# Kernel tuning notes

Hardware: AMD Instinct MI355X
Metric: run time of the kernel (lower is better)

Reference implementation:

```python
import jax, jax.numpy as jnp
import numpy as np

D = 64  # hidden_dim


def _bn(x, gamma, beta):
    # eval-mode BatchNorm1d with running_mean=0, running_var=1 (fresh model)
    return gamma * x + beta


def _edge_conv(h, W, b, gamma, beta):
    # h: [B,N,D]; W: [2D,D] split into Wi (acts on x_i) and Wj (acts on x_j)
    Wi, Wj = W[:D], W[D:]
    ti = jnp.einsum('bnd,de->bne', h, Wi)  # [B,N,D] (i term)
    tj = jnp.einsum('bmd,de->bme', h, Wj)  # [B,N,D] (j term)
    # e[b,i,j,:] = x_i@Wi + x_j@Wj + b  -> relu -> BN -> max over j
    e = ti[:, :, None, :] + tj[:, None, :, :] + b  # [B,N,N,D]
    e = _bn(jax.nn.relu(e), gamma, beta)
    return e.max(axis=2)  # [B,N,D]


def setup_inputs() -> dict:
    key = jax.random.key(0)
    ks = jax.random.split(key, 16)
    s = lambda k, shp, sc: (jax.random.normal(k, shp, dtype=jnp.float32) * sc)
    inp = {
        'x': s(ks[0], (32, 256, 4), 1.0),
        'W1': s(ks[1], (4, D), 0.5), 'b1': s(ks[2], (D,), 0.1),
        'g1': 1.0 + s(ks[3], (D,), 0.1), 'beta1': s(ks[4], (D,), 0.1),
        'We1': s(ks[5], (2 * D, D), 0.1), 'be1': s(ks[6], (D,), 0.1),
        'ge1': 1.0 + s(ks[7], (D,), 0.1), 'betae1': s(ks[8], (D,), 0.1),
        'We2': s(ks[9], (2 * D, D), 0.1), 'be2': s(ks[10], (D,), 0.1),
        'ge2': 1.0 + s(ks[11], (D,), 0.1), 'betae2': s(ks[12], (D,), 0.1),
        'Wg1': s(ks[13], (2 * D, D), 0.1), 'bg1': s(ks[14], (D,), 0.1),
        'Wg2': s(ks[15], (D, 2), 0.1), 'bg2': jnp.zeros((2,), jnp.float32),
    }
    return inp


def reference(x, W1, b1, g1, beta1, We1, be1, ge1, betae1, We2, be2, ge2, betae2, Wg1, bg1, Wg2, bg2):
    # input MLP: Linear -> ReLU -> BN (eval)
    h = _bn(jax.nn.relu(x @ W1 + b1), g1, beta1)  # [B,N,D]
    h = _edge_conv(h, We1, be1, ge1, betae1)
    h = _edge_conv(h, We2, be2, ge2, betae2)
    x_mean = h.mean(axis=1)  # [B,D]
    x_max = h.max(axis=1)    # [B,D]
    xg = jnp.concatenate([x_mean, x_max], axis=-1)  # [B,2D]
    # global MLP (dropout is identity in eval)
    out = jax.nn.relu(xg @ Wg1 + bg1) @ Wg2 + bg2  # [B,2]
    return out
```

## Files before the change

### kernel.cpp

```cpp
#include <hip/hip_runtime.h>

#define NB 32
#define NN 256
#define DD 64
#define GG 4
#define NPB 64
#define FMAXV 3.402823466e+38f


__global__ __launch_bounds__(512) void k_conv1(
    const float* __restrict__ x,
    const float* __restrict__ W1,  const float* __restrict__ b1,
    const float* __restrict__ g1,  const float* __restrict__ beta1,
    const float* __restrict__ We1,
    float* __restrict__ TI, float* __restrict__ PMAX, float* __restrict__ PMIN)
{
    __shared__ float Hs[NPB * 65];
    const int b  = blockIdx.x >> 2;
    const int g  = blockIdx.x & 3;
    const int l  = threadIdx.x & 63;
    const int w  = __builtin_amdgcn_readfirstlane(threadIdx.x >> 6);
    const int n  = g * NPB + l;
    const int d0 = w * 8;

    {
        float4 xv = *(const float4*)(x + ((size_t)b * NN + n) * 4);
        float a[8];
#pragma unroll
        for (int j = 0; j < 8; ++j) a[j] = b1[d0 + j];
#pragma unroll
        for (int j = 0; j < 8; ++j) a[j] = fmaf(xv.x, W1[0 * DD + d0 + j], a[j]);
#pragma unroll
        for (int j = 0; j < 8; ++j) a[j] = fmaf(xv.y, W1[1 * DD + d0 + j], a[j]);
#pragma unroll
        for (int j = 0; j < 8; ++j) a[j] = fmaf(xv.z, W1[2 * DD + d0 + j], a[j]);
#pragma unroll
        for (int j = 0; j < 8; ++j) a[j] = fmaf(xv.w, W1[3 * DD + d0 + j], a[j]);
#pragma unroll
        for (int j = 0; j < 8; ++j)
            Hs[l * 65 + d0 + j] = g1[d0 + j] * fmaxf(a[j], 0.f) + beta1[d0 + j];
    }
    __syncthreads();

    float ti[8], tj[8];
#pragma unroll
    for (int j = 0; j < 8; ++j) { ti[j] = 0.f; tj[j] = 0.f; }
#pragma unroll
    for (int k = 0; k < DD; ++k) {
        const float hk = Hs[l * 65 + k];
        const float* wi = We1 + k * DD + d0;
        const float* wj = We1 + (DD + k) * DD + d0;
#pragma unroll
        for (int j = 0; j < 8; ++j) {
            ti[j] = fmaf(hk, wi[j], ti[j]);
            tj[j] = fmaf(hk, wj[j], tj[j]);
        }
    }
    {
        float* o = TI + ((size_t)(b * NN + n)) * DD + d0;
        *(float4*)(o)     = make_float4(ti[0], ti[1], ti[2], ti[3]);
        *(float4*)(o + 4) = make_float4(ti[4], ti[5], ti[6], ti[7]);
    }
    float mx[8], mn[8];
#pragma unroll
    for (int j = 0; j < 8; ++j) { mx[j] = tj[j]; mn[j] = tj[j]; }
#pragma unroll
    for (int m = 1; m < 64; m <<= 1) {
#pragma unroll
        for (int j = 0; j < 8; ++j) {
            mx[j] = fmaxf(mx[j], __shfl_xor(mx[j], m, 64));
            mn[j] = fminf(mn[j], __shfl_xor(mn[j], m, 64));
        }
    }
    float smx = mx[0], smn = mn[0];
#pragma unroll
    for (int j = 1; j < 8; ++j) {
        smx = (l == j) ? mx[j] : smx;
        smn = (l == j) ? mn[j] : smn;
    }
    if (l < 8) {
        PMAX[(b * GG + g) * DD + d0 + l] = smx;
        PMIN[(b * GG + g) * DD + d0 + l] = smn;
    }
}

__global__ __launch_bounds__(512) void k_conv2(
    const float* __restrict__ PMAXin, const float* __restrict__ PMINin,
    const float* __restrict__ beP, const float* __restrict__ geP,
    const float* __restrict__ bteP,
    const float* __restrict__ We,
    float* __restrict__ TI, float* __restrict__ PMAX, float* __restrict__ PMIN)
{
    __shared__ float Hs[NPB * 65];
    const int b  = blockIdx.x >> 2;
    const int g  = blockIdx.x & 3;
    const int l  = threadIdx.x & 63;
    const int w  = __builtin_amdgcn_readfirstlane(threadIdx.x >> 6);
    const int n  = g * NPB + l;
    const int d0 = w * 8;

    float rmax[8], rmin[8];
#pragma unroll
    for (int j = 0; j < 8; ++j) {
        rmax[j] = fmaxf(fmaxf(PMAXin[(b * GG + 0) * DD + d0 + j],
                              PMAXin[(b * GG + 1) * DD + d0 + j]),
                        fmaxf(PMAXin[(b * GG + 2) * DD + d0 + j],
                              PMAXin[(b * GG + 3) * DD + d0 + j]));
        rmin[j] = fminf(fminf(PMINin[(b * GG + 0) * DD + d0 + j],
                              PMINin[(b * GG + 1) * DD + d0 + j]),
                        fminf(PMINin[(b * GG + 2) * DD + d0 + j],
                              PMINin[(b * GG + 3) * DD + d0 + j]));
    }
    {
        const float* tip = TI + ((size_t)(b * NN + n)) * DD + d0;
        float4 t0 = *(const float4*)tip;
        float4 t1 = *(const float4*)(tip + 4);
        float tiv[8] = {t0.x, t0.y, t0.z, t0.w, t1.x, t1.y, t1.z, t1.w};
#pragma unroll
        for (int j = 0; j < 8; ++j) {
            float gv = geP[d0 + j];
            float sv = tiv[j] + (gv >= 0.f ? rmax[j] : rmin[j]) + beP[d0 + j];
            Hs[l * 65 + d0 + j] = gv * fmaxf(sv, 0.f) + bteP[d0 + j];
        }
    }
    __syncthreads();

    float ti[8], tj[8];
#pragma unroll
    for (int j = 0; j < 8; ++j) { ti[j] = 0.f; tj[j] = 0.f; }
#pragma unroll
    for (int k = 0; k < DD; ++k) {
        const float hk = Hs[l * 65 + k];
        const float* wi = We + k * DD + d0;
        const float* wj = We + (DD + k) * DD + d0;
#pragma unroll
        for (int j = 0; j < 8; ++j) {
            ti[j] = fmaf(hk, wi[j], ti[j]);
            tj[j] = fmaf(hk, wj[j], tj[j]);
        }
    }
    {
        float* o = TI + ((size_t)(b * NN + n)) * DD + d0;
        *(float4*)(o)     = make_float4(ti[0], ti[1], ti[2], ti[3]);
        *(float4*)(o + 4) = make_float4(ti[4], ti[5], ti[6], ti[7]);
    }
    float mx[8], mn[8];
#pragma unroll
    for (int j = 0; j < 8; ++j) { mx[j] = tj[j]; mn[j] = tj[j]; }
#pragma unroll
    for (int m = 1; m < 64; m <<= 1) {
#pragma unroll
        for (int j = 0; j < 8; ++j) {
            mx[j] = fmaxf(mx[j], __shfl_xor(mx[j], m, 64));
            mn[j] = fminf(mn[j], __shfl_xor(mn[j], m, 64));
        }
    }
    float smx = mx[0], smn = mn[0];
#pragma unroll
    for (int j = 1; j < 8; ++j) {
        smx = (l == j) ? mx[j] : smx;
        smn = (l == j) ? mn[j] : smn;
    }
    if (l < 8) {
        PMAX[(b * GG + g) * DD + d0 + l] = smx;
        PMIN[(b * GG + g) * DD + d0 + l] = smn;
    }
}

__global__ __launch_bounds__(512) void k_pool(
    const float* __restrict__ PMAXin, const float* __restrict__ PMINin,
    const float* __restrict__ beP, const float* __restrict__ geP,
    const float* __restrict__ bteP,
    const float* __restrict__ TI,
    float* __restrict__ PSUM, float* __restrict__ PMXP)
{
    const int b  = blockIdx.x >> 2;
    const int g  = blockIdx.x & 3;
    const int l  = threadIdx.x & 63;
    const int w  = __builtin_amdgcn_readfirstlane(threadIdx.x >> 6);
    const int n  = g * NPB + l;
    const int d0 = w * 8;

    float rmax[8], rmin[8];
#pragma unroll
    for (int j = 0; j < 8; ++j) {
        rmax[j] = fmaxf(fmaxf(PMAXin[(b * GG + 0) * DD + d0 + j],
                              PMAXin[(b * GG + 1) * DD + d0 + j]),
                        fmaxf(PMAXin[(b * GG + 2) * DD + d0 + j],
                              PMAXin[(b * GG + 3) * DD + d0 + j]));
        rmin[j] = fminf(fminf(PMINin[(b * GG + 0) * DD + d0 + j],
                              PMINin[(b * GG + 1) * DD + d0 + j]),
                        fminf(PMINin[(b * GG + 2) * DD + d0 + j],
                              PMINin[(b * GG + 3) * DD + d0 + j]));
    }
    float hv[8];
    {
        const float* tip = TI + ((size_t)(b * NN + n)) * DD + d0;
        float4 t0 = *(const float4*)tip;
        float4 t1 = *(const float4*)(tip + 4);
        float tiv[8] = {t0.x, t0.y, t0.z, t0.w, t1.x, t1.y, t1.z, t1.w};
#pragma unroll
        for (int j = 0; j < 8; ++j) {
            float gv = geP[d0 + j];
            float sv = tiv[j] + (gv >= 0.f ? rmax[j] : rmin[j]) + beP[d0 + j];
            hv[j] = gv * fmaxf(sv, 0.f) + bteP[d0 + j];
        }
    }
    float sm[8], mx[8];
#pragma unroll
    for (int j = 0; j < 8; ++j) { sm[j] = hv[j]; mx[j] = hv[j]; }
#pragma unroll
    for (int m = 1; m < 64; m <<= 1) {
#pragma unroll
        for (int j = 0; j < 8; ++j) {
            sm[j] += __shfl_xor(sm[j], m, 64);
            mx[j] = fmaxf(mx[j], __shfl_xor(mx[j], m, 64));
        }
    }
    float ssm = sm[0], smx = mx[0];
#pragma unroll
    for (int j = 1; j < 8; ++j) {
        ssm = (l == j) ? sm[j] : ssm;
        smx = (l == j) ? mx[j] : smx;
    }
    if (l < 8) {
        PSUM[(b * GG + g) * DD + d0 + l] = ssm;
        PMXP[(b * GG + g) * DD + d0 + l] = smx;
    }
}

__global__ __launch_bounds__(128) void k_head(
    const float* __restrict__ PSUM, const float* __restrict__ PMXP,
    const float* __restrict__ Wg1, const float* __restrict__ bg1,
    const float* __restrict__ Wg2, const float* __restrict__ bg2,
    float* __restrict__ out)
{
    __shared__ float xg[2 * DD];
    __shared__ float hid[DD];
    const int b = blockIdx.x;
    const int t = threadIdx.x;
    if (t < 64) {
        float s = PSUM[(b * GG + 0) * DD + t] + PSUM[(b * GG + 1) * DD + t]
                + PSUM[(b * GG + 2) * DD + t] + PSUM[(b * GG + 3) * DD + t];
        xg[t] = s * (1.f / 256.f);
    } else {
        int d = t - 64;
        xg[64 + d] = fmaxf(fmaxf(PMXP[(b * GG + 0) * DD + d], PMXP[(b * GG + 1) * DD + d]),
                           fmaxf(PMXP[(b * GG + 2) * DD + d], PMXP[(b * GG + 3) * DD + d]));
    }
    __syncthreads();
    if (t < 64) {
        float a = bg1[t];
#pragma unroll
        for (int k = 0; k < 2 * DD; ++k) a = fmaf(xg[k], Wg1[k * DD + t], a);
        hid[t] = fmaxf(a, 0.f);
    }
    __syncthreads();
    if (t < 2) {
        float o = bg2[t];
#pragma unroll
        for (int j = 0; j < DD; ++j) o = fmaf(hid[j], Wg2[j * 2 + t], o);
        out[b * 2 + t] = o;
    }
}

extern "C" void kernel_launch(void* const* d_in, const int* in_sizes, int n_in,
                              void* d_out, int out_size, void* d_ws, size_t ws_size,
                              hipStream_t stream) {
    const float* x     = (const float*)d_in[0];
    const float* W1    = (const float*)d_in[1];
    const float* b1    = (const float*)d_in[2];
    const float* g1    = (const float*)d_in[3];
    const float* beta1 = (const float*)d_in[4];
    const float* We1   = (const float*)d_in[5];
    const float* be1   = (const float*)d_in[6];
    const float* ge1   = (const float*)d_in[7];
    const float* bte1  = (const float*)d_in[8];
    const float* We2   = (const float*)d_in[9];
    const float* be2   = (const float*)d_in[10];
    const float* ge2   = (const float*)d_in[11];
    const float* bte2  = (const float*)d_in[12];
    const float* Wg1   = (const float*)d_in[13];
    const float* bg1   = (const float*)d_in[14];
    const float* Wg2   = (const float*)d_in[15];
    const float* bg2   = (const float*)d_in[16];

    float* ws    = (float*)d_ws;
    float* TI    = ws;
    float* PMAX1 = ws + 524288;
    float* PMIN1 = ws + 532480;
    float* PMAX2 = ws + 540672;
    float* PMIN2 = ws + 548864;
    float* PSUM  = ws + 557056;
    float* PMXP  = ws + 565248;

    k_conv1<<<dim3(NB * GG), dim3(512), 0, stream>>>(
        x, W1, b1, g1, beta1, We1, TI, PMAX1, PMIN1);
    k_conv2<<<dim3(NB * GG), dim3(512), 0, stream>>>(
        PMAX1, PMIN1, be1, ge1, bte1, We2, TI, PMAX2, PMIN2);
    k_pool<<<dim3(NB * GG), dim3(512), 0, stream>>>(
        PMAX2, PMIN2, be2, ge2, bte2, TI, PSUM, PMXP);
    k_head<<<dim3(NB), dim3(128), 0, stream>>>(
        PSUM, PMXP, Wg1, bg1, Wg2, bg2, (float*)d_out);
}
```

Before: 121.3 us.

## Fuse all stages into one cooperative kernel with grid-wide syncs

Replaces the four kernel launches (conv1, conv2, pool, head) with a single cooperative kernel that separates stages with grid.sync(). The ti values now stay in registers between stages, so the TI round-trip through global memory is gone, and the head runs in the g==0 blocks. This removes launch gaps and global traffic. In exchange it pays for grid-barrier costs, needs all 128 blocks co-resident, and leaves 3/4 of the blocks idle during the head.

```diff
diff --git a/kernel.cpp b/kernel.cpp
--- a/kernel.cpp
+++ b/kernel.cpp
@@ -1,27 +1,89 @@
 #include <hip/hip_runtime.h>
+#include <hip/hip_cooperative_groups.h>
+
+namespace cg = cooperative_groups;
 
 #define NB 32
 #define NN 256
 #define DD 64
 #define GG 4
 #define NPB 64
-#define FMAXV 3.402823466e+38f
-
-
-__global__ __launch_bounds__(512) void k_conv1(
+
+
+__device__ __forceinline__ void matvec64(const float* Hrow, int d0,
+                                         const float* __restrict__ We,
+                                         float ti[8], float tj[8])
+{
+#pragma unroll
+    for (int j = 0; j < 8; ++j) { ti[j] = 0.f; tj[j] = 0.f; }
+#pragma unroll
+    for (int k = 0; k < DD; ++k) {
+        const float hk = Hrow[k];
+        const float* wi = We + k * DD + d0;
+        const float* wj = We + (DD + k) * DD + d0;
+#pragma unroll
+        for (int j = 0; j < 8; ++j) {
+            ti[j] = fmaf(hk, wi[j], ti[j]);
+            tj[j] = fmaf(hk, wj[j], tj[j]);
+        }
+    }
+}
+
+__device__ __forceinline__ void red_minmax_store(const float tj[8], int l,
+                                                 float* PMAX, float* PMIN, int idx)
+{
+    float mx[8], mn[8];
+#pragma unroll
+    for (int j = 0; j < 8; ++j) { mx[j] = tj[j]; mn[j] = tj[j]; }
+#pragma unroll
+    for (int m = 1; m < 64; m <<= 1) {
+#pragma unroll
+        for (int j = 0; j < 8; ++j) {
+            mx[j] = fmaxf(mx[j], __shfl_xor(mx[j], m, 64));
+            mn[j] = fminf(mn[j], __shfl_xor(mn[j], m, 64));
+        }
+    }
+    float smx = mx[0], smn = mn[0];
+#pragma unroll
+    for (int j = 1; j < 8; ++j) {
+        smx = (l == j) ? mx[j] : smx;
+        smn = (l == j) ? mn[j] : smn;
+    }
+    if (l < 8) {
+        PMAX[idx + l] = smx;
+        PMIN[idx + l] = smn;
+    }
+}
+
+__global__ __launch_bounds__(512, 2) void k_fused(
     const float* __restrict__ x,
     const float* __restrict__ W1,  const float* __restrict__ b1,
     const float* __restrict__ g1,  const float* __restrict__ beta1,
-    const float* __restrict__ We1,
-    float* __restrict__ TI, float* __restrict__ PMAX, float* __restrict__ PMIN)
+    const float* __restrict__ We1, const float* __restrict__ be1,
+    const float* __restrict__ ge1, const float* __restrict__ bte1,
+    const float* __restrict__ We2, const float* __restrict__ be2,
+    const float* __restrict__ ge2, const float* __restrict__ bte2,
+    const float* __restrict__ Wg1, const float* __restrict__ bg1,
+    const float* __restrict__ Wg2, const float* __restrict__ bg2,
+    float* ws, float* __restrict__ out)
 {
+    cg::grid_group grid = cg::this_grid();
     __shared__ float Hs[NPB * 65];
+
+    float* PMAX1 = ws;
+    float* PMIN1 = ws + 8192;
+    float* PMAX2 = ws + 16384;
+    float* PMIN2 = ws + 24576;
+    float* PSUM  = ws + 32768;
+    float* PMXP  = ws + 40960;
+
     const int b  = blockIdx.x >> 2;
     const int g  = blockIdx.x & 3;
     const int l  = threadIdx.x & 63;
     const int w  = __builtin_amdgcn_readfirstlane(threadIdx.x >> 6);
     const int n  = g * NPB + l;
     const int d0 = w * 8;
+    const int pidx = (b * GG + g) * DD + d0;
 
     {
         float4 xv = *(const float4*)(x + ((size_t)b * NN + n) * 4);
@@ -43,224 +105,104 @@
     __syncthreads();
 
     float ti[8], tj[8];
-#pragma unroll
-    for (int j = 0; j < 8; ++j) { ti[j] = 0.f; tj[j] = 0.f; }
-#pragma unroll
-    for (int k = 0; k < DD; ++k) {
-        const float hk = Hs[l * 65 + k];
-        const float* wi = We1 + k * DD + d0;
-        const float* wj = We1 + (DD + k) * DD + d0;
-#pragma unroll
-        for (int j = 0; j < 8; ++j) {
-            ti[j] = fmaf(hk, wi[j], ti[j]);
-            tj[j] = fmaf(hk, wj[j], tj[j]);
-        }
-    }
+    matvec64(Hs + l * 65, d0, We1, ti, tj);
+    red_minmax_store(tj, l, PMAX1, PMIN1, pidx);
+
+    grid.sync();
+
     {
-        float* o = TI + ((size_t)(b * NN + n)) * DD + d0;
-        *(float4*)(o)     = make_float4(ti[0], ti[1], ti[2], ti[3]);
-        *(float4*)(o + 4) = make_float4(ti[4], ti[5], ti[6], ti[7]);
-    }
-    float mx[8], mn[8];
-#pragma unroll
-    for (int j = 0; j < 8; ++j) { mx[j] = tj[j]; mn[j] = tj[j]; }
-#pragma unroll
-    for (int m = 1; m < 64; m <<= 1) {
-#pragma unroll
-        for (int j = 0; j < 8; ++j) {
-            mx[j] = fmaxf(mx[j], __shfl_xor(mx[j], m, 64));
-            mn[j] = fminf(mn[j], __shfl_xor(mn[j], m, 64));
-        }
-    }
-    float smx = mx[0], smn = mn[0];
-#pragma unroll
-    for (int j = 1; j < 8; ++j) {
-        smx = (l == j) ? mx[j] : smx;
-        smn = (l == j) ? mn[j] : smn;
-    }
-    if (l < 8) {
-        PMAX[(b * GG + g) * DD + d0 + l] = smx;
-        PMIN[(b * GG + g) * DD + d0 + l] = smn;
-    }
-}
-
-__global__ __launch_bounds__(512) void k_conv2(
-    const float* __restrict__ PMAXin, const float* __restrict__ PMINin,
-    const float* __restrict__ beP, const float* __restrict__ geP,
-    const float* __restrict__ bteP,
-    const float* __restrict__ We,
-    float* __restrict__ TI, float* __restrict__ PMAX, float* __restrict__ PMIN)
-{
-    __shared__ float Hs[NPB * 65];
-    const int b  = blockIdx.x >> 2;
-    const int g  = blockIdx.x & 3;
-    const int l  = threadIdx.x & 63;
-    const int w  = __builtin_amdgcn_readfirstlane(threadIdx.x >> 6);
-    const int n  = g * NPB + l;
-    const int d0 = w * 8;
-
-    float rmax[8], rmin[8];
-#pragma unroll
-    for (int j = 0; j < 8; ++j) {
-        rmax[j] = fmaxf(fmaxf(PMAXin[(b * GG + 0) * DD + d0 + j],
-                              PMAXin[(b * GG + 1) * DD + d0 + j]),
-                        fmaxf(PMAXin[(b * GG + 2) * DD + d0 + j],
-                              PMAXin[(b * GG + 3) * DD + d0 + j]));
-        rmin[j] = fminf(fminf(PMINin[(b * GG + 0) * DD + d0 + j],
-                              PMINin[(b * GG + 1) * DD + d0 + j]),
-                        fminf(PMINin[(b * GG + 2) * DD + d0 + j],
-                              PMINin[(b * GG + 3) * DD + d0 + j]));
-    }
+        float rmax[8], rmin[8];
+#pragma unroll
+        for (int j = 0; j < 8; ++j) {
+            const int base = b * GG * DD + d0 + j;
+            rmax[j] = fmaxf(fmaxf(PMAX1[base],          PMAX1[base + DD]),
+                            fmaxf(PMAX1[base + 2 * DD], PMAX1[base + 3 * DD]));
+            rmin[j] = fminf(fminf(PMIN1[base],          PMIN1[base + DD]),
+                            fminf(PMIN1[base + 2 * DD], PMIN1[base + 3 * DD]));
+        }
+#pragma unroll
+        for (int j = 0; j < 8; ++j) {
+            float gv = ge1[d0 + j];
+            float sv = ti[j] + (gv >= 0.f ? rmax[j] : rmin[j]) + be1[d0 + j];
+            Hs[l * 65 + d0 + j] = gv * fmaxf(sv, 0.f) + bte1[d0 + j];
+        }
+    }
+    __syncthreads();
+
+    matvec64(Hs + l * 65, d0, We2, ti, tj);
+    red_minmax_store(tj, l, PMAX2, PMIN2, pidx);
+
+    grid.sync();
+
     {
-        const float* tip = TI + ((size_t)(b * NN + n)) * DD + d0;
-        float4 t0 = *(const float4*)tip;
-        float4 t1 = *(const float4*)(tip + 4);
-        float tiv[8] = {t0.x, t0.y, t0.z, t0.w, t1.x, t1.y, t1.z, t1.w};
-#pragma unroll
-        for (int j = 0; j < 8; ++j) {
-            float gv = geP[d0 + j];
-            float sv = tiv[j] + (gv >= 0.f ? rmax[j] : rmin[j]) + beP[d0 + j];
-            Hs[l * 65 + d0 + j] = gv * fmaxf(sv, 0.f) + bteP[d0 + j];
-        }
-    }
-    __syncthreads();
-
-    float ti[8], tj[8];
-#pragma unroll
-    for (int j = 0; j < 8; ++j) { ti[j] = 0.f; tj[j] = 0.f; }
-#pragma unroll
-    for (int k = 0; k < DD; ++k) {
-        const float hk = Hs[l * 65 + k];
-        const float* wi = We + k * DD + d0;
-        const float* wj = We + (DD + k) * DD + d0;
-#pragma unroll
-        for (int j = 0; j < 8; ++j) {
-            ti[j] = fmaf(hk, wi[j], ti[j]);
-            tj[j] = fmaf(hk, wj[j], tj[j]);
-        }
-    }
-    {
-        float* o = TI + ((size_t)(b * NN + n)) * DD + d0;
-        *(float4*)(o)     = make_float4(ti[0], ti[1], ti[2], ti[3]);
-        *(float4*)(o + 4) = make_float4(ti[4], ti[5], ti[6], ti[7]);
-    }
-    float mx[8], mn[8];
-#pragma unroll
-    for (int j = 0; j < 8; ++j) { mx[j] = tj[j]; mn[j] = tj[j]; }
-#pragma unroll
-    for (int m = 1; m < 64; m <<= 1) {
-#pragma unroll
-        for (int j = 0; j < 8; ++j) {
-            mx[j] = fmaxf(mx[j], __shfl_xor(mx[j], m, 64));
-            mn[j] = fminf(mn[j], __shfl_xor(mn[j], m, 64));
-        }
-    }
-    float smx = mx[0], smn = mn[0];
-#pragma unroll
-    for (int j = 1; j < 8; ++j) {
-        smx = (l == j) ? mx[j] : smx;
-        smn = (l == j) ? mn[j] : smn;
-    }
-    if (l < 8) {
-        PMAX[(b * GG + g) * DD + d0 + l] = smx;
-        PMIN[(b * GG + g) * DD + d0 + l] = smn;
-    }
-}
-
-__global__ __launch_bounds__(512) void k_pool(
-    const float* __restrict__ PMAXin, const float* __restrict__ PMINin,
-    const float* __restrict__ beP, const float* __restrict__ geP,
-    const float* __restrict__ bteP,
-    const float* __restrict__ TI,
-    float* __restrict__ PSUM, float* __restrict__ PMXP)
-{
-    const int b  = blockIdx.x >> 2;
-    const int g  = blockIdx.x & 3;
-    const int l  = threadIdx.x & 63;
-    const int w  = __builtin_amdgcn_readfirstlane(threadIdx.x >> 6);
-    const int n  = g * NPB + l;
-    const int d0 = w * 8;
-
-    float rmax[8], rmin[8];
-#pragma unroll
-    for (int j = 0; j < 8; ++j) {
-        rmax[j] = fmaxf(fmaxf(PMAXin[(b * GG + 0) * DD + d0 + j],
-                              PMAXin[(b * GG + 1) * DD + d0 + j]),
-                        fmaxf(PMAXin[(b * GG + 2) * DD + d0 + j],
-                              PMAXin[(b * GG + 3) * DD + d0 + j]));
-        rmin[j] = fminf(fminf(PMINin[(b * GG + 0) * DD + d0 + j],
-                              PMINin[(b * GG + 1) * DD + d0 + j]),
-                        fminf(PMINin[(b * GG + 2) * DD + d0 + j],
-                              PMINin[(b * GG + 3) * DD + d0 + j]));
-    }
-    float hv[8];
-    {
-        const float* tip = TI + ((size_t)(b * NN + n)) * DD + d0;
-        float4 t0 = *(const float4*)tip;
-        float4 t1 = *(const float4*)(tip + 4);
-        float tiv[8] = {t0.x, t0.y, t0.z, t0.w, t1.x, t1.y, t1.z, t1.w};
-#pragma unroll
-        for (int j = 0; j < 8; ++j) {
-            float gv = geP[d0 + j];
-            float sv = tiv[j] + (gv >= 0.f ? rmax[j] : rmin[j]) + beP[d0 + j];
-            hv[j] = gv * fmaxf(sv, 0.f) + bteP[d0 + j];
-        }
-    }
-    float sm[8], mx[8];
-#pragma unroll
-    for (int j = 0; j < 8; ++j) { sm[j] = hv[j]; mx[j] = hv[j]; }
-#pragma unroll
-    for (int m = 1; m < 64; m <<= 1) {
-#pragma unroll
-        for (int j = 0; j < 8; ++j) {
-            sm[j] += __shfl_xor(sm[j], m, 64);
-            mx[j] = fmaxf(mx[j], __shfl_xor(mx[j], m, 64));
-        }
-    }
-    float ssm = sm[0], smx = mx[0];
-#pragma unroll
-    for (int j = 1; j < 8; ++j) {
-        ssm = (l == j) ? sm[j] : ssm;
-        smx = (l == j) ? mx[j] : smx;
-    }
-    if (l < 8) {
-        PSUM[(b * GG + g) * DD + d0 + l] = ssm;
-        PMXP[(b * GG + g) * DD + d0 + l] = smx;
-    }
-}
-
-__global__ __launch_bounds__(128) void k_head(
-    const float* __restrict__ PSUM, const float* __restrict__ PMXP,
-    const float* __restrict__ Wg1, const float* __restrict__ bg1,
-    const float* __restrict__ Wg2, const float* __restrict__ bg2,
-    float* __restrict__ out)
-{
-    __shared__ float xg[2 * DD];
-    __shared__ float hid[DD];
-    const int b = blockIdx.x;
-    const int t = threadIdx.x;
-    if (t < 64) {
-        float s = PSUM[(b * GG + 0) * DD + t] + PSUM[(b * GG + 1) * DD + t]
-                + PSUM[(b * GG + 2) * DD + t] + PSUM[(b * GG + 3) * DD + t];
-        xg[t] = s * (1.f / 256.f);
-    } else {
-        int d = t - 64;
-        xg[64 + d] = fmaxf(fmaxf(PMXP[(b * GG + 0) * DD + d], PMXP[(b * GG + 1) * DD + d]),
-                           fmaxf(PMXP[(b * GG + 2) * DD + d], PMXP[(b * GG + 3) * DD + d]));
-    }
-    __syncthreads();
-    if (t < 64) {
-        float a = bg1[t];
-#pragma unroll
-        for (int k = 0; k < 2 * DD; ++k) a = fmaf(xg[k], Wg1[k * DD + t], a);
-        hid[t] = fmaxf(a, 0.f);
-    }
-    __syncthreads();
-    if (t < 2) {
-        float o = bg2[t];
-#pragma unroll
-        for (int j = 0; j < DD; ++j) o = fmaf(hid[j], Wg2[j * 2 + t], o);
-        out[b * 2 + t] = o;
+        float rmax[8], rmin[8];
+#pragma unroll
+        for (int j = 0; j < 8; ++j) {
+            const int base = b * GG * DD + d0 + j;
+            rmax[j] = fmaxf(fmaxf(PMAX2[base],          PMAX2[base + DD]),
+                            fmaxf(PMAX2[base + 2 * DD], PMAX2[base + 3 * DD]));
+            rmin[j] = fminf(fminf(PMIN2[base],          PMIN2[base + DD]),
+                            fminf(PMIN2[base + 2 * DD], PMIN2[base + 3 * DD]));
+        }
+        float hv[8];
+#pragma unroll
+        for (int j = 0; j < 8; ++j) {
+            float gv = ge2[d0 + j];
+            float sv = ti[j] + (gv >= 0.f ? rmax[j] : rmin[j]) + be2[d0 + j];
+            hv[j] = gv * fmaxf(sv, 0.f) + bte2[d0 + j];
+        }
+        float sm[8], mx[8];
+#pragma unroll
+        for (int j = 0; j < 8; ++j) { sm[j] = hv[j]; mx[j] = hv[j]; }
+#pragma unroll
+        for (int m = 1; m < 64; m <<= 1) {
+#pragma unroll
+            for (int j = 0; j < 8; ++j) {
+                sm[j] += __shfl_xor(sm[j], m, 64);
+                mx[j] = fmaxf(mx[j], __shfl_xor(mx[j], m, 64));
+            }
+        }
+        float ssm = sm[0], smx = mx[0];
+#pragma unroll
+        for (int j = 1; j < 8; ++j) {
+            ssm = (l == j) ? sm[j] : ssm;
+            smx = (l == j) ? mx[j] : smx;
+        }
+        if (l < 8) {
+            PSUM[pidx + l] = ssm;
+            PMXP[pidx + l] = smx;
+        }
+    }
+
+    grid.sync();
+
+    if (g == 0) {
+        const int t = threadIdx.x;
+        float* xg  = Hs;
+        float* hid = Hs + 128;
+        if (t < 64) {
+            float s = PSUM[(b * GG + 0) * DD + t] + PSUM[(b * GG + 1) * DD + t]
+                    + PSUM[(b * GG + 2) * DD + t] + PSUM[(b * GG + 3) * DD + t];
+            xg[t] = s * (1.f / 256.f);
+        } else if (t < 128) {
+            int d = t - 64;
+            xg[64 + d] = fmaxf(fmaxf(PMXP[(b * GG + 0) * DD + d], PMXP[(b * GG + 1) * DD + d]),
+                               fmaxf(PMXP[(b * GG + 2) * DD + d], PMXP[(b * GG + 3) * DD + d]));
+        }
+        __syncthreads();
+        if (t < 64) {
+            float a = bg1[t];
+#pragma unroll
+            for (int k = 0; k < 2 * DD; ++k) a = fmaf(xg[k], Wg1[k * DD + t], a);
+            hid[t] = fmaxf(a, 0.f);
+        }
+        __syncthreads();
+        if (t < 2) {
+            float o = bg2[t];
+#pragma unroll
+            for (int j = 0; j < DD; ++j) o = fmaf(hid[j], Wg2[j * 2 + t], o);
+            out[b * 2 + t] = o;
+        }
     }
 }
 
@@ -284,22 +226,15 @@
     const float* bg1   = (const float*)d_in[14];
     const float* Wg2   = (const float*)d_in[15];
     const float* bg2   = (const float*)d_in[16];
-
-    float* ws    = (float*)d_ws;
-    float* TI    = ws;
-    float* PMAX1 = ws + 524288;
-    float* PMIN1 = ws + 532480;
-    float* PMAX2 = ws + 540672;
-    float* PMIN2 = ws + 548864;
-    float* PSUM  = ws + 557056;
-    float* PMXP  = ws + 565248;
-
-    k_conv1<<<dim3(NB * GG), dim3(512), 0, stream>>>(
-        x, W1, b1, g1, beta1, We1, TI, PMAX1, PMIN1);
-    k_conv2<<<dim3(NB * GG), dim3(512), 0, stream>>>(
-        PMAX1, PMIN1, be1, ge1, bte1, We2, TI, PMAX2, PMIN2);
-    k_pool<<<dim3(NB * GG), dim3(512), 0, stream>>>(
-        PMAX2, PMIN2, be2, ge2, bte2, TI, PSUM, PMXP);
-    k_head<<<dim3(NB), dim3(128), 0, stream>>>(
-        PSUM, PMXP, Wg1, bg1, Wg2, bg2, (float*)d_out);
-}
+    float* ws   = (float*)d_ws;
+    float* outp = (float*)d_out;
+
+    void* args[] = { &x, &W1, &b1, &g1, &beta1,
+                     &We1, &be1, &ge1, &bte1,
+                     &We2, &be2, &ge2, &bte2,
+                     &Wg1, &bg1, &Wg2, &bg2,
+                     &ws, &outp };
+
+    hipLaunchCooperativeKernel((const void*)k_fused, dim3(NB * GG), dim3(512),
+                               args, 0, stream);
+}
```

New measurement: 203.9 us. +68.1%, slower.

## Fuse pooling and head into conv2 via last-block atomic counter

Applied to the files above, without the earlier changes.

Merges the pooling and global-MLP head kernels into the second conv kernel. Each batch's four blocks bump a per-batch atomic counter, and the last block to arrive reduces the partial max/min, pools over all 256 points and runs the head MLP. This removes two kernel launches and the PSUM/PMXP round trip through global memory. The cost is threadfence/atomic synchronization and a serialized tail done by a single block per batch.

```diff
diff --git a/kernel.cpp b/kernel.cpp
--- a/kernel.cpp
+++ b/kernel.cpp
@@ -13,7 +13,8 @@
     const float* __restrict__ W1,  const float* __restrict__ b1,
     const float* __restrict__ g1,  const float* __restrict__ beta1,
     const float* __restrict__ We1,
-    float* __restrict__ TI, float* __restrict__ PMAX, float* __restrict__ PMIN)
+    float* __restrict__ TI, float* __restrict__ PMAX, float* __restrict__ PMIN,
+    int* __restrict__ CNT)
 {
     __shared__ float Hs[NPB * 65];
     const int b  = blockIdx.x >> 2;
@@ -23,6 +24,8 @@
     const int n  = g * NPB + l;
     const int d0 = w * 8;
 
+    if (g == 0 && threadIdx.x == 0) CNT[b] = 0;
+
     {
         float4 xv = *(const float4*)(x + ((size_t)b * NN + n) * 4);
         float a[8];
@@ -84,14 +87,20 @@
     }
 }
 
-__global__ __launch_bounds__(512) void k_conv2(
-    const float* __restrict__ PMAXin, const float* __restrict__ PMINin,
-    const float* __restrict__ beP, const float* __restrict__ geP,
-    const float* __restrict__ bteP,
+__global__ __launch_bounds__(512) void k_conv2_tail(
+    const float* PMAXin, const float* PMINin,
+    const float* __restrict__ be1P, const float* __restrict__ ge1P,
+    const float* __restrict__ bte1P,
     const float* __restrict__ We,
-    float* __restrict__ TI, float* __restrict__ PMAX, float* __restrict__ PMIN)
+    const float* __restrict__ be2P, const float* __restrict__ ge2P,
+    const float* __restrict__ bte2P,
+    const float* __restrict__ Wg1, const float* __restrict__ bg1,
+    const float* __restrict__ Wg2, const float* __restrict__ bg2,
+    float* TI, float* PMAX, float* PMIN, int* CNT,
+    float* __restrict__ out)
 {
     __shared__ float Hs[NPB * 65];
+    __shared__ int amLast;
     const int b  = blockIdx.x >> 2;
     const int g  = blockIdx.x & 3;
     const int l  = threadIdx.x & 63;
@@ -102,14 +111,11 @@
     float rmax[8], rmin[8];
 #pragma unroll
     for (int j = 0; j < 8; ++j) {
-        rmax[j] = fmaxf(fmaxf(PMAXin[(b * GG + 0) * DD + d0 + j],
-                              PMAXin[(b * GG + 1) * DD + d0 + j]),
-                        fmaxf(PMAXin[(b * GG + 2) * DD + d0 + j],
-                              PMAXin[(b * GG + 3) * DD + d0 + j]));
-        rmin[j] = fminf(fminf(PMINin[(b * GG + 0) * DD + d0 + j],
-                              PMINin[(b * GG + 1) * DD + d0 + j]),
-                        fminf(PMINin[(b * GG + 2) * DD + d0 + j],
-                              PMINin[(b * GG + 3) * DD + d0 + j]));
+        const int base = b * GG * DD + d0 + j;
+        rmax[j] = fmaxf(fmaxf(PMAXin[base],          PMAXin[base + DD]),
+                        fmaxf(PMAXin[base + 2 * DD], PMAXin[base + 3 * DD]));
+        rmin[j] = fminf(fminf(PMINin[base],          PMINin[base + DD]),
+                        fminf(PMINin[base + 2 * DD], PMINin[base + 3 * DD]));
     }
     {
         const float* tip = TI + ((size_t)(b * NN + n)) * DD + d0;
@@ -118,9 +124,9 @@
         float tiv[8] = {t0.x, t0.y, t0.z, t0.w, t1.x, t1.y, t1.z, t1.w};
 #pragma unroll
         for (int j = 0; j < 8; ++j) {
-            float gv = geP[d0 + j];
-            float sv = tiv[j] + (gv >= 0.f ? rmax[j] : rmin[j]) + beP[d0 + j];
-            Hs[l * 65 + d0 + j] = gv * fmaxf(sv, 0.f) + bteP[d0 + j];
+            float gv = ge1P[d0 + j];
+            float sv = tiv[j] + (gv >= 0.f ? rmax[j] : rmin[j]) + be1P[d0 + j];
+            Hs[l * 65 + d0 + j] = gv * fmaxf(sv, 0.f) + bte1P[d0 + j];
         }
     }
     __syncthreads();
@@ -165,90 +171,69 @@
         PMAX[(b * GG + g) * DD + d0 + l] = smx;
         PMIN[(b * GG + g) * DD + d0 + l] = smn;
     }
-}
-
-__global__ __launch_bounds__(512) void k_pool(
-    const float* __restrict__ PMAXin, const float* __restrict__ PMINin,
-    const float* __restrict__ beP, const float* __restrict__ geP,
-    const float* __restrict__ bteP,
-    const float* __restrict__ TI,
-    float* __restrict__ PSUM, float* __restrict__ PMXP)
-{
-    const int b  = blockIdx.x >> 2;
-    const int g  = blockIdx.x & 3;
-    const int l  = threadIdx.x & 63;
-    const int w  = __builtin_amdgcn_readfirstlane(threadIdx.x >> 6);
-    const int n  = g * NPB + l;
-    const int d0 = w * 8;
-
-    float rmax[8], rmin[8];
+
+    __threadfence();
+    __syncthreads();
+    if (threadIdx.x == 0) {
+        int old = atomicAdd(&CNT[b], 1);
+        amLast = (old == GG - 1);
+    }
+    __syncthreads();
+    if (!amLast) return;
+
+    __threadfence();
+
+    float rmax2[8], rmin2[8];
 #pragma unroll
     for (int j = 0; j < 8; ++j) {
-        rmax[j] = fmaxf(fmaxf(PMAXin[(b * GG + 0) * DD + d0 + j],
-                              PMAXin[(b * GG + 1) * DD + d0 + j]),
-                        fmaxf(PMAXin[(b * GG + 2) * DD + d0 + j],
-                              PMAXin[(b * GG + 3) * DD + d0 + j]));
-        rmin[j] = fminf(fminf(PMINin[(b * GG + 0) * DD + d0 + j],
-                              PMINin[(b * GG + 1) * DD + d0 + j]),
-                        fminf(PMINin[(b * GG + 2) * DD + d0 + j],
-                              PMINin[(b * GG + 3) * DD + d0 + j]));
-    }
-    float hv[8];
-    {
-        const float* tip = TI + ((size_t)(b * NN + n)) * DD + d0;
+        const int base = b * GG * DD + d0 + j;
+        rmax2[j] = fmaxf(fmaxf(PMAX[base],          PMAX[base + DD]),
+                         fmaxf(PMAX[base + 2 * DD], PMAX[base + 3 * DD]));
+        rmin2[j] = fminf(fminf(PMIN[base],          PMIN[base + DD]),
+                         fminf(PMIN[base + 2 * DD], PMIN[base + 3 * DD]));
+    }
+    float sm[8], mxp[8];
+#pragma unroll
+    for (int j = 0; j < 8; ++j) { sm[j] = 0.f; mxp[j] = -FMAXV; }
+#pragma unroll
+    for (int c = 0; c < 4; ++c) {
+        const int n2 = c * 64 + l;
+        const float* tip = TI + ((size_t)(b * NN + n2)) * DD + d0;
         float4 t0 = *(const float4*)tip;
         float4 t1 = *(const float4*)(tip + 4);
         float tiv[8] = {t0.x, t0.y, t0.z, t0.w, t1.x, t1.y, t1.z, t1.w};
 #pragma unroll
         for (int j = 0; j < 8; ++j) {
-            float gv = geP[d0 + j];
-            float sv = tiv[j] + (gv >= 0.f ? rmax[j] : rmin[j]) + beP[d0 + j];
-            hv[j] = gv * fmaxf(sv, 0.f) + bteP[d0 + j];
-        }
-    }
-    float sm[8], mx[8];
-#pragma unroll
-    for (int j = 0; j < 8; ++j) { sm[j] = hv[j]; mx[j] = hv[j]; }
+            float gv = ge2P[d0 + j];
+            float sv = tiv[j] + (gv >= 0.f ? rmax2[j] : rmin2[j]) + be2P[d0 + j];
+            float hv = gv * fmaxf(sv, 0.f) + bte2P[d0 + j];
+            sm[j] += hv;
+            mxp[j] = fmaxf(mxp[j], hv);
+        }
+    }
 #pragma unroll
     for (int m = 1; m < 64; m <<= 1) {
 #pragma unroll
         for (int j = 0; j < 8; ++j) {
             sm[j] += __shfl_xor(sm[j], m, 64);
-            mx[j] = fmaxf(mx[j], __shfl_xor(mx[j], m, 64));
-        }
-    }
-    float ssm = sm[0], smx = mx[0];
+            mxp[j] = fmaxf(mxp[j], __shfl_xor(mxp[j], m, 64));
+        }
+    }
+    float ssm = sm[0], smxp = mxp[0];
 #pragma unroll
     for (int j = 1; j < 8; ++j) {
-        ssm = (l == j) ? sm[j] : ssm;
-        smx = (l == j) ? mx[j] : smx;
-    }
+        ssm  = (l == j) ? sm[j]  : ssm;
+        smxp = (l == j) ? mxp[j] : smxp;
+    }
+    float* xg  = Hs;
+    float* hid = Hs + 128;
+    __syncthreads();
     if (l < 8) {
-        PSUM[(b * GG + g) * DD + d0 + l] = ssm;
-        PMXP[(b * GG + g) * DD + d0 + l] = smx;
-    }
-}
-
-__global__ __launch_bounds__(128) void k_head(
-    const float* __restrict__ PSUM, const float* __restrict__ PMXP,
-    const float* __restrict__ Wg1, const float* __restrict__ bg1,
-    const float* __restrict__ Wg2, const float* __restrict__ bg2,
-    float* __restrict__ out)
-{
-    __shared__ float xg[2 * DD];
-    __shared__ float hid[DD];
-    const int b = blockIdx.x;
+        xg[d0 + l]      = ssm * (1.f / 256.f);
+        xg[64 + d0 + l] = smxp;
+    }
+    __syncthreads();
     const int t = threadIdx.x;
-    if (t < 64) {
-        float s = PSUM[(b * GG + 0) * DD + t] + PSUM[(b * GG + 1) * DD + t]
-                + PSUM[(b * GG + 2) * DD + t] + PSUM[(b * GG + 3) * DD + t];
-        xg[t] = s * (1.f / 256.f);
-    } else {
-        int d = t - 64;
-        xg[64 + d] = fmaxf(fmaxf(PMXP[(b * GG + 0) * DD + d], PMXP[(b * GG + 1) * DD + d]),
-                           fmaxf(PMXP[(b * GG + 2) * DD + d], PMXP[(b * GG + 3) * DD + d]));
-    }
-    __syncthreads();
     if (t < 64) {
         float a = bg1[t];
 #pragma unroll
@@ -291,15 +276,11 @@
     float* PMIN1 = ws + 532480;
     float* PMAX2 = ws + 540672;
     float* PMIN2 = ws + 548864;
-    float* PSUM  = ws + 557056;
-    float* PMXP  = ws + 565248;
+    int*   CNT   = (int*)(ws + 557056);
 
     k_conv1<<<dim3(NB * GG), dim3(512), 0, stream>>>(
-        x, W1, b1, g1, beta1, We1, TI, PMAX1, PMIN1);
-    k_conv2<<<dim3(NB * GG), dim3(512), 0, stream>>>(
-        PMAX1, PMIN1, be1, ge1, bte1, We2, TI, PMAX2, PMIN2);
-    k_pool<<<dim3(NB * GG), dim3(512), 0, stream>>>(
-        PMAX2, PMIN2, be2, ge2, bte2, TI, PSUM, PMXP);
-    k_head<<<dim3(NB), dim3(128), 0, stream>>>(
-        PSUM, PMXP, Wg1, bg1, Wg2, bg2, (float*)d_out);
+        x, W1, b1, g1, beta1, We1, TI, PMAX1, PMIN1, CNT);
+    k_conv2_tail<<<dim3(NB * GG), dim3(512), 0, stream>>>(
+        PMAX1, PMIN1, be1, ge1, bte1, We2, be2, ge2, bte2,
+        Wg1, bg1, Wg2, bg2, TI, PMAX2, PMIN2, CNT, (float*)d_out);
 }
```

New measurement: 151.6 us. +25.0%, slower.
